# Performance work log

Hardware: AMD Instinct MI355X
Metric: run time of the kernel (lower is better)

## Reference

```python
import jax, jax.numpy as jnp
import numpy as np

M, K1, N1, N2, N3 = 131072, 256, 1024, 1024, 256


def setup_inputs() -> dict:
    key = jax.random.key(0)
    k_x, k1, k2, k3 = jax.random.split(key, 4)
    x = jax.random.normal(k_x, (M, K1), dtype=jnp.float32)
    # Kaiming-ish scaling so softplus stays in a sane range
    w1 = jax.random.normal(k1, (K1, N1), dtype=jnp.float32) * (1.0 / np.sqrt(K1))
    w2 = jax.random.normal(k2, (N1, N2), dtype=jnp.float32) * (1.0 / np.sqrt(N1))
    w3 = jax.random.normal(k3, (N2, N3), dtype=jnp.float32) * (1.0 / np.sqrt(N2))
    return {"x": x, "w1": w1, "w2": w2, "w3": w3}


def reference(x, w1, w2, w3):
    # Fused 3-layer MLP: out = softplus(softplus(x @ W1) @ W2) @ W3
    h1 = jax.nn.softplus(x @ w1)   # [M, N1]
    h2 = jax.nn.softplus(h1 @ w2)  # [M, N2]
    return h2 @ w3                 # [M, N3]
```

## Files before the change

### kernel.cpp

```cpp
#include <hip/hip_runtime.h>

typedef __attribute__((ext_vector_type(8))) short short8;
typedef __attribute__((ext_vector_type(4))) float floatx4;
typedef __attribute__((ext_vector_type(2))) unsigned int uintx2;
typedef __attribute__((ext_vector_type(4))) unsigned int uintx4;
typedef unsigned short u16;

#define MFMA(a, b, c) __builtin_amdgcn_mfma_f32_16x16x32_bf16((a), (b), (c), 0, 0, 0)
#define BAR() do { asm volatile("" ::: "memory"); __builtin_amdgcn_s_barrier(); \
                   asm volatile("" ::: "memory"); } while (0)
#define LGKM0() asm volatile("s_waitcnt lgkmcnt(0)" ::: "memory")

__device__ __forceinline__ u16 f2bf(float f) {
  unsigned int u = __builtin_bit_cast(unsigned int, f);
  u += ((u >> 16) & 1u) + 0x7fffu;
  return (u16)(u >> 16);
}

__device__ __forceinline__ float softplus_f(float v) {
  float a = __builtin_fabsf(v);
  float e = __expf(-a);
  float l = __logf(1.0f + e);
  return __builtin_fmaxf(v, 0.0f) + l;
}

__device__ __forceinline__ unsigned int pack_sp(float lo, float hi) {
  return (unsigned int)f2bf(softplus_f(lo)) | ((unsigned int)f2bf(softplus_f(hi)) << 16);
}

__global__ void transpose_cvt(const float* __restrict__ in, u16* __restrict__ out, int K, int N) {
  __shared__ float tile[32][33];
  const int bn = blockIdx.x * 32, bk = blockIdx.y * 32;
  const int tx = threadIdx.x, ty = threadIdx.y;
#pragma unroll
  for (int i = 0; i < 32; i += 8)
    tile[ty + i][tx] = in[(size_t)(bk + ty + i) * N + bn + tx];
  __syncthreads();
#pragma unroll
  for (int i = 0; i < 32; i += 8)
    out[(size_t)(bn + ty + i) * K + bk + tx] = f2bf(tile[tx][ty + i]);
}

__device__ __forceinline__ void gld16(const void* g, void* l) {
  __builtin_amdgcn_global_load_lds((const __attribute__((address_space(1))) void*)g,
                                   (__attribute__((address_space(3))) void*)l, 16, 0, 0);
}

template <int K, int EPI, bool ACTF32>
__global__ __launch_bounds__(512, 2) void gemm8(const void* __restrict__ actv,
                                                const u16* __restrict__ wt,
                                                void* __restrict__ Cout, int N, int nbn) {
  constexpr int H = K / 64;
  __shared__ u16 lds[2 * 4 * 8192];
  u16* L = lds;
  const int tid = threadIdx.x, lane = tid & 63, wv = tid >> 6;
  const int l15 = lane & 15, g = lane >> 4;
  const int wvm = wv >> 2, wvn = wv & 3;
  const int nwg = gridDim.x, o = blockIdx.x;
  const int sw = (o & 7) * (nwg >> 3) + (o >> 3);
  const int bm = sw / nbn, bn = sw % nbn;
  const size_t am0 = (size_t)bm * 256;
  const size_t wn0 = (size_t)bn * 256;

  int afo[8], wfo[4];
#pragma unroll
  for (int mt = 0; mt < 8; ++mt) {
    const int r = mt * 16 + l15;
    afo[mt] = (r * 8 + (g ^ ((r >> 1) & 7))) * 8;
  }
#pragma unroll
  for (int nt = 0; nt < 4; ++nt) {
    const int r = (wvn & 1) * 64 + nt * 16 + l15;
    wfo[nt] = (r * 8 + (g ^ ((r >> 1) & 7))) * 8;
  }
  const int aHalf = wvm * 8192;
  const int wHalf = (2 + (wvn >> 1)) * 8192;

  int soff[2], sdst[2];
#pragma unroll
  for (int j = 0; j < 2; ++j) {
    const int s = j * 512 + tid;
    const int r = s >> 3, gg = (s & 7) ^ ((r >> 1) & 7);
    soff[j] = r * K + gg * 8;
    sdst[j] = s * 8;
  }
  const u16* actb = nullptr;
  const float* factb = nullptr;
  if constexpr (ACTF32) factb = (const float*)actv + am0 * K;
  else actb = (const u16*)actv + am0 * K;
  const u16* wtb = wt + wn0 * K;

#define STG_W(tt, hi)                                                                \
  { _Pragma("unroll") for (int j = 0; j < 2; ++j)                                    \
      gld16(wtb + (size_t)(hi)*128 * K + soff[j] + (tt)*64,                          \
            L + ((tt)&1) * 32768 + (2 + (hi)) * 8192 + sdst[j]); }
#define STG_AB(tt, hi)                                                               \
  { _Pragma("unroll") for (int j = 0; j < 2; ++j)                                    \
      gld16(actb + (size_t)(hi)*128 * K + soff[j] + (tt)*64,                         \
            L + ((tt)&1) * 32768 + (hi)*8192 + sdst[j]); }
#define STG_AF(tt, hi)                                                               \
  { floatx4 v0[2], v1[2];                                                            \
    _Pragma("unroll") for (int j = 0; j < 2; ++j) {                                  \
      const float* sp_ = factb + (size_t)(hi)*128 * K + soff[j] + (tt)*64;           \
      v0[j] = *(const floatx4*)sp_;                                                  \
      v1[j] = *(const floatx4*)(sp_ + 4);                                            \
    }                                                                                \
    _Pragma("unroll") for (int j = 0; j < 2; ++j) {                                  \
      uintx4 w_;                                                                     \
      w_.x = (unsigned)f2bf(v0[j].x) | ((unsigned)f2bf(v0[j].y) << 16);              \
      w_.y = (unsigned)f2bf(v0[j].z) | ((unsigned)f2bf(v0[j].w) << 16);              \
      w_.z = (unsigned)f2bf(v1[j].x) | ((unsigned)f2bf(v1[j].y) << 16);              \
      w_.w = (unsigned)f2bf(v1[j].z) | ((unsigned)f2bf(v1[j].w) << 16);              \
      *(uintx4*)(L + ((tt)&1) * 32768 + (hi)*8192 + sdst[j]) = w_;                   \
    } }
#define STG_A(tt, hi)                                                                \
  { if constexpr (ACTF32) STG_AF(tt, hi) else STG_AB(tt, hi) }

  floatx4 acc[4][8];
  const floatx4 z4 = {0.f, 0.f, 0.f, 0.f};
#pragma unroll
  for (int t = 0; t < 4; ++t)
#pragma unroll
    for (int mt = 0; mt < 8; ++mt) acc[t][mt] = z4;

  STG_W(0, 0) STG_W(0, 1) STG_A(0, 0) STG_A(0, 1)
  STG_A(1, 0) STG_A(1, 1)
  if constexpr (ACTF32) { asm volatile("s_waitcnt vmcnt(0)" ::: "memory"); LGKM0(); }
  else asm volatile("s_waitcnt vmcnt(4)" ::: "memory");
  BAR();

  short8 A0[8], A1[8], wf0, wf1;

#pragma unroll 1
  for (int t = 0; t < H; ++t) {
    const int cb = (t & 1) * 32768;
#pragma unroll
    for (int mt = 0; mt < 8; ++mt) A0[mt] = *(const short8*)(L + cb + aHalf + afo[mt]);
    wf0 = *(const short8*)(L + cb + wHalf + wfo[0]);
    wf1 = *(const short8*)(L + cb + wHalf + wfo[1]);
    if (t + 1 < H) STG_W(t + 1, 0)
    BAR(); LGKM0();
    __builtin_amdgcn_s_setprio(1);
#pragma unroll
    for (int mt = 0; mt < 8; ++mt) {
      acc[0][mt] = MFMA(wf0, A0[mt], acc[0][mt]);
      acc[1][mt] = MFMA(wf1, A0[mt], acc[1][mt]);
    }
    __builtin_amdgcn_s_setprio(0);
    BAR();
#pragma unroll
    for (int mt = 0; mt < 8; ++mt) A1[mt] = *(const short8*)(L + cb + aHalf + (afo[mt] ^ 32));
    wf0 = *(const short8*)(L + cb + wHalf + (wfo[0] ^ 32));
    wf1 = *(const short8*)(L + cb + wHalf + (wfo[1] ^ 32));
    if (t + 1 < H) STG_W(t + 1, 1)
    BAR(); LGKM0();
    __builtin_amdgcn_s_setprio(1);
#pragma unroll
    for (int mt = 0; mt < 8; ++mt) {
      acc[0][mt] = MFMA(wf0, A1[mt], acc[0][mt]);
      acc[1][mt] = MFMA(wf1, A1[mt], acc[1][mt]);
    }
    __builtin_amdgcn_s_setprio(0);
    BAR();
    wf0 = *(const short8*)(L + cb + wHalf + wfo[2]);
    wf1 = *(const short8*)(L + cb + wHalf + wfo[3]);
    if (t + 2 < H) STG_A(t + 2, 0)
    BAR(); LGKM0();
    __builtin_amdgcn_s_setprio(1);
#pragma unroll
    for (int mt = 0; mt < 8; ++mt) {
      acc[2][mt] = MFMA(wf0, A0[mt], acc[2][mt]);
      acc[3][mt] = MFMA(wf1, A0[mt], acc[3][mt]);
    }
    __builtin_amdgcn_s_setprio(0);
    BAR();
    wf0 = *(const short8*)(L + cb + wHalf + (wfo[2] ^ 32));
    wf1 = *(const short8*)(L + cb + wHalf + (wfo[3] ^ 32));
    if (t + 2 < H) STG_A(t + 2, 1)
    if (t < H - 2) asm volatile("s_waitcnt vmcnt(4)" ::: "memory");
    else if (t == H - 2) asm volatile("s_waitcnt vmcnt(0)" ::: "memory");
    BAR(); LGKM0();
    __builtin_amdgcn_s_setprio(1);
#pragma unroll
    for (int mt = 0; mt < 8; ++mt) {
      acc[2][mt] = MFMA(wf0, A1[mt], acc[2][mt]);
      acc[3][mt] = MFMA(wf1, A1[mt], acc[3][mt]);
    }
    __builtin_amdgcn_s_setprio(0);
    BAR();
  }
#undef STG_W
#undef STG_AB
#undef STG_AF
#undef STG_A

  __syncthreads();

  if constexpr (EPI == 0) {
    u16* cl = L;
#pragma unroll
    for (int t = 0; t < 4; ++t)
#pragma unroll
      for (int mt = 0; mt < 8; ++mt) {
        const int m = wvm * 128 + mt * 16 + l15;
        const int n0 = wvn * 64 + t * 16 + g * 4;
        const int j = n0 >> 3, hh = (n0 >> 2) & 1;
        uintx2 pk;
        pk.x = pack_sp(acc[t][mt].x, acc[t][mt].y);
        pk.y = pack_sp(acc[t][mt].z, acc[t][mt].w);
        *(uintx2*)(cl + m * 256 + ((j ^ (m & 7)) << 3) + (hh << 2)) = pk;
      }
    __syncthreads();
    u16* outp = (u16*)Cout;
#pragma unroll
    for (int i = 0; i < 16; ++i) {
      const int c = i * 512 + tid;
      const int m = c >> 5, j = c & 31;
      uintx4 v = *(const uintx4*)(cl + m * 256 + ((j ^ (m & 7)) << 3));
      *(uintx4*)(outp + (am0 + m) * N + wn0 + j * 8) = v;
    }
  } else {
    float* cf = (float*)L;
#pragma unroll
    for (int q = 0; q < 2; ++q) {
      if (q) __syncthreads();
      if (wvm == q) {
#pragma unroll
        for (int t = 0; t < 4; ++t)
#pragma unroll
          for (int mt = 0; mt < 8; ++mt) {
            const int m = mt * 16 + l15;
            const int p = (wvn * 64 + t * 16 + g * 4) >> 1;
            *(floatx4*)(cf + m * 256 + ((p ^ ((m & 7) << 1)) << 1)) = acc[t][mt];
          }
      }
      __syncthreads();
      float* outp = (float*)Cout;
#pragma unroll
      for (int i = 0; i < 16; ++i) {
        const int c = i * 512 + tid;
        const int m = c >> 6, cc = c & 63;
        const int p = cc * 2;
        floatx4 v = *(const floatx4*)(cf + m * 256 + ((p ^ ((m & 7) << 1)) << 1));
        *(floatx4*)(outp + (am0 + q * 128 + m) * N + wn0 + cc * 4) = v;
      }
    }
  }
}

__global__ __launch_bounds__(512, 2) void mlp3_fused(const float* __restrict__ x,
                                                     const u16* __restrict__ w1t,
                                                     const u16* __restrict__ w2t,
                                                     const u16* __restrict__ w3t,
                                                     float* __restrict__ out) {
  __shared__ u16 h1s[64 * 1024];
  __shared__ u16 xs[64 * 256];
  const int tid = threadIdx.x, lane = tid & 63, wv = tid >> 6;
  const int l15 = lane & 15, g = lane >> 4;
  const size_t m0 = (size_t)blockIdx.x * 64;
  const floatx4 z4 = {0.f, 0.f, 0.f, 0.f};
  {
    const float* xp = x + m0 * 256;
#pragma unroll
    for (int r = 0; r < 8; ++r) {
      int idx4 = r * 512 + tid;
      int m = idx4 >> 6, k = (idx4 & 63) << 2;
      floatx4 v = *(const floatx4*)(xp + m * 256 + k);
      uintx2 pk;
      pk.x = (unsigned)f2bf(v.x) | ((unsigned)f2bf(v.y) << 16);
      pk.y = (unsigned)f2bf(v.z) | ((unsigned)f2bf(v.w) << 16);
      *(uintx2*)(xs + ((m * 256 + k) ^ ((m & 7) << 3))) = pk;
    }
  }
  __syncthreads();
#pragma unroll 1
  for (int c = 0; c < 4; ++c) {
    floatx4 acc[2][4];
#pragma unroll
    for (int t = 0; t < 2; ++t)
#pragma unroll
      for (int mt = 0; mt < 4; ++mt) acc[t][mt] = z4;
    const u16* p0 = w1t + (size_t)(c * 256 + wv * 32 + l15) * 256;
#pragma unroll
    for (int ks = 0; ks < 8; ++ks) {
      const int k = ks * 32 + g * 8;
      short8 a0 = *(const short8*)(p0 + k);
      short8 a1 = *(const short8*)(p0 + 16 * 256 + k);
      short8 b0 = *(const short8*)(xs + (((0 * 16 + l15) * 256 + k) ^ ((l15 & 7) << 3)));
      short8 b1 = *(const short8*)(xs + (((1 * 16 + l15) * 256 + k) ^ ((l15 & 7) << 3)));
      short8 b2 = *(const short8*)(xs + (((2 * 16 + l15) * 256 + k) ^ ((l15 & 7) << 3)));
      short8 b3 = *(const short8*)(xs + (((3 * 16 + l15) * 256 + k) ^ ((l15 & 7) << 3)));
      acc[0][0] = MFMA(a0, b0, acc[0][0]); acc[0][1] = MFMA(a0, b1, acc[0][1]);
      acc[0][2] = MFMA(a0, b2, acc[0][2]); acc[0][3] = MFMA(a0, b3, acc[0][3]);
      acc[1][0] = MFMA(a1, b0, acc[1][0]); acc[1][1] = MFMA(a1, b1, acc[1][1]);
      acc[1][2] = MFMA(a1, b2, acc[1][2]); acc[1][3] = MFMA(a1, b3, acc[1][3]);
    }
#pragma unroll
    for (int t = 0; t < 2; ++t)
#pragma unroll
      for (int mt = 0; mt < 4; ++mt) {
        const int n1 = c * 256 + wv * 32 + t * 16 + g * 4;
        const int m = mt * 16 + l15;
        uintx2 pk;
        pk.x = pack_sp(acc[t][mt].x, acc[t][mt].y);
        pk.y = pack_sp(acc[t][mt].z, acc[t][mt].w);
        *(uintx2*)(h1s + ((m * 1024 + n1) ^ ((m & 7) << 3))) = pk;
      }
  }
  __syncthreads();
  floatx4 acc3[2][4];
#pragma unroll
  for (int t = 0; t < 2; ++t)
#pragma unroll
    for (int mt = 0; mt < 4; ++mt) acc3[t][mt] = z4;
#pragma unroll 1
  for (int c2 = 0; c2 < 4; ++c2) {
    floatx4 acc2[2][4];
#pragma unroll
    for (int t = 0; t < 2; ++t)
#pragma unroll
      for (int mt = 0; mt < 4; ++mt) acc2[t][mt] = z4;
    {
      const u16* p0 = w2t + (size_t)(c2 * 256 + wv * 32 + l15) * 1024;
#pragma unroll 4
      for (int ks = 0; ks < 32; ++ks) {
        const int k = ks * 32 + g * 8;
        short8 a0 = *(const short8*)(p0 + k);
        short8 a1 = *(const short8*)(p0 + 16 * 1024 + k);
        short8 b0 = *(const short8*)(h1s + (((0 * 16 + l15) * 1024 + k) ^ ((l15 & 7) << 3)));
        short8 b1 = *(const short8*)(h1s + (((1 * 16 + l15) * 1024 + k) ^ ((l15 & 7) << 3)));
        short8 b2 = *(const short8*)(h1s + (((2 * 16 + l15) * 1024 + k) ^ ((l15 & 7) << 3)));
        short8 b3 = *(const short8*)(h1s + (((3 * 16 + l15) * 1024 + k) ^ ((l15 & 7) << 3)));
        acc2[0][0] = MFMA(a0, b0, acc2[0][0]); acc2[0][1] = MFMA(a0, b1, acc2[0][1]);
        acc2[0][2] = MFMA(a0, b2, acc2[0][2]); acc2[0][3] = MFMA(a0, b3, acc2[0][3]);
        acc2[1][0] = MFMA(a1, b0, acc2[1][0]); acc2[1][1] = MFMA(a1, b1, acc2[1][1]);
        acc2[1][2] = MFMA(a1, b2, acc2[1][2]); acc2[1][3] = MFMA(a1, b3, acc2[1][3]);
      }
    }
    __syncthreads();
#pragma unroll
    for (int t = 0; t < 2; ++t)
#pragma unroll
      for (int mt = 0; mt < 4; ++mt) {
        const int n2l = wv * 32 + t * 16 + g * 4;
        const int m = mt * 16 + l15;
        uintx2 pk;
        pk.x = pack_sp(acc2[t][mt].x, acc2[t][mt].y);
        pk.y = pack_sp(acc2[t][mt].z, acc2[t][mt].w);
        *(uintx2*)(xs + ((m * 256 + n2l) ^ ((m & 7) << 3))) = pk;
      }
    __syncthreads();
    {
      const u16* p0 = w3t + (size_t)(wv * 32 + l15) * 1024 + c2 * 256;
#pragma unroll
      for (int ks = 0; ks < 8; ++ks) {
        const int k = ks * 32 + g * 8;
        short8 a0 = *(const short8*)(p0 + k);
        short8 a1 = *(const short8*)(p0 + 16 * 1024 + k);
        short8 b0 = *(const short8*)(xs + (((0 * 16 + l15) * 256 + k) ^ ((l15 & 7) << 3)));
        short8 b1 = *(const short8*)(xs + (((1 * 16 + l15) * 256 + k) ^ ((l15 & 7) << 3)));
        short8 b2 = *(const short8*)(xs + (((2 * 16 + l15) * 256 + k) ^ ((l15 & 7) << 3)));
        short8 b3 = *(const short8*)(xs + (((3 * 16 + l15) * 256 + k) ^ ((l15 & 7) << 3)));
        acc3[0][0] = MFMA(a0, b0, acc3[0][0]); acc3[0][1] = MFMA(a0, b1, acc3[0][1]);
        acc3[0][2] = MFMA(a0, b2, acc3[0][2]); acc3[0][3] = MFMA(a0, b3, acc3[0][3]);
        acc3[1][0] = MFMA(a1, b0, acc3[1][0]); acc3[1][1] = MFMA(a1, b1, acc3[1][1]);
        acc3[1][2] = MFMA(a1, b2, acc3[1][2]); acc3[1][3] = MFMA(a1, b3, acc3[1][3]);
      }
    }
  }
#pragma unroll
  for (int t = 0; t < 2; ++t)
#pragma unroll
    for (int mt = 0; mt < 4; ++mt) {
      const int n3 = wv * 32 + t * 16 + g * 4;
      const int m = mt * 16 + l15;
      *(floatx4*)(out + (m0 + m) * 256 + n3) = acc3[t][mt];
    }
}

extern "C" void kernel_launch(void* const* d_in, const int* in_sizes, int n_in,
                              void* d_out, int out_size, void* d_ws, size_t ws_size,
                              hipStream_t stream) {
  const float* x = (const float*)d_in[0];
  const float* w1 = (const float*)d_in[1];
  const float* w2 = (const float*)d_in[2];
  const float* w3 = (const float*)d_in[3];
  float* out = (float*)d_out;
  const size_t M = 131072;

  u16* w1t = (u16*)d_ws;
  u16* w2t = w1t + 1024 * 256;
  u16* w3t = w2t + 1024 * 1024;
  u16* bufA = w3t + 256 * 1024;
  const size_t weights_el = 1024 * 256 + 1024 * 1024 + 256 * 1024;

  size_t CM = 0;
  const size_t cands[4] = {32768, 16384, 8192, 4096};
  for (int i = 0; i < 4; ++i) {
    size_t need = (weights_el + 2 * cands[i] * 1024) * sizeof(u16);
    if (ws_size >= need) { CM = cands[i]; break; }
  }

  dim3 tb(32, 8);
  transpose_cvt<<<dim3(32, 8), tb, 0, stream>>>(w1, w1t, 256, 1024);
  transpose_cvt<<<dim3(32, 32), tb, 0, stream>>>(w2, w2t, 1024, 1024);
  transpose_cvt<<<dim3(8, 32), tb, 0, stream>>>(w3, w3t, 1024, 256);

  if (CM) {
    u16* bufB = bufA + CM * 1024;
    const int nchunk = (int)(M / CM);
    for (int ci = 0; ci < nchunk; ++ci) {
      const float* xc = x + (size_t)ci * CM * 256;
      float* oc = out + (size_t)ci * CM * 256;
      gemm8<256, 0, true><<<(int)(CM / 256) * 4, 512, 0, stream>>>(xc, w1t, bufA, 1024, 4);
      gemm8<1024, 0, false><<<(int)(CM / 256) * 4, 512, 0, stream>>>(bufA, w2t, bufB, 1024, 4);
      gemm8<1024, 1, false><<<(int)(CM / 256), 512, 0, stream>>>(bufB, w3t, oc, 256, 1);
    }
  } else {
    mlp3_fused<<<M / 64, 512, 0, stream>>>(x, w1t, w2t, w3t, out);
  }
}
```

Baseline: 708.7 us.

## Store activations and weights as pre-swizzled tile images for contiguous LDS staging

Weights and intermediate activations are rewritten into a tiled layout that matches the swizzled LDS order, so each GEMM stage copies contiguous 16KB blocks straight into LDS. The fp32-to-bf16 conversion of x moves out of the first GEMM into a separate cvt_ximg pass, and GEMM epilogues now write the next layer's tile layout directly. The goal is fully coalesced, direct global-to-LDS loads and a simpler load path. The cost is an extra conversion kernel per chunk, extra x write/read traffic, and more setup kernels for the weights.

Result: no change. 713.6 us (+0.7%).

```diff
diff --git a/kernel.cpp b/kernel.cpp
--- a/kernel.cpp
+++ b/kernel.cpp
@@ -41,15 +41,50 @@
     out[(size_t)(bn + ty + i) * K + bk + tx] = f2bf(tile[tx][ty + i]);
 }
 
+
+__global__ void make_wimg(const u16* __restrict__ wt, u16* __restrict__ img, int K, int H) {
+  const int b = blockIdx.x;
+  const int hi = b & 1, th = (b >> 1) % H, bn = (b >> 1) / H;
+  const int tid = threadIdx.x;
+#pragma unroll
+  for (int j = 0; j < 2; ++j) {
+    const int s = j * 512 + tid;
+    const int r = s >> 3, gg = s & 7;
+    const int k0 = th * 64 + ((gg ^ ((r >> 1) & 7)) << 3);
+    short8 v = *(const short8*)(wt + (size_t)(bn * 256 + hi * 128 + r) * K + k0);
+    *(short8*)(img + (size_t)b * 8192 + s * 8) = v;
+  }
+}
+
+__global__ void cvt_ximg(const float* __restrict__ x, u16* __restrict__ img) {
+  const int b = blockIdx.x;
+  const int hi = b & 1, th = (b >> 1) & 3, mi = b >> 3;
+  const int tid = threadIdx.x;
+#pragma unroll
+  for (int j = 0; j < 2; ++j) {
+    const int s = j * 512 + tid;
+    const int r = s >> 3, gg = s & 7;
+    const int k0 = th * 64 + ((gg ^ ((r >> 1) & 7)) << 3);
+    const float* p = x + (size_t)(mi * 256 + hi * 128 + r) * 256 + k0;
+    floatx4 a = *(const floatx4*)p, c = *(const floatx4*)(p + 4);
+    uintx4 w;
+    w.x = (unsigned)f2bf(a.x) | ((unsigned)f2bf(a.y) << 16);
+    w.y = (unsigned)f2bf(a.z) | ((unsigned)f2bf(a.w) << 16);
+    w.z = (unsigned)f2bf(c.x) | ((unsigned)f2bf(c.y) << 16);
+    w.w = (unsigned)f2bf(c.z) | ((unsigned)f2bf(c.w) << 16);
+    *(uintx4*)(img + (size_t)b * 8192 + s * 8) = w;
+  }
+}
+
 __device__ __forceinline__ void gld16(const void* g, void* l) {
   __builtin_amdgcn_global_load_lds((const __attribute__((address_space(1))) void*)g,
                                    (__attribute__((address_space(3))) void*)l, 16, 0, 0);
 }
 
-template <int K, int EPI, bool ACTF32>
-__global__ __launch_bounds__(512, 2) void gemm8(const void* __restrict__ actv,
-                                                const u16* __restrict__ wt,
-                                                void* __restrict__ Cout, int N, int nbn) {
+template <int K, int HOUT, int EPI>
+__global__ __launch_bounds__(512, 2) void gemm8i(const u16* __restrict__ actimg,
+                                                 const u16* __restrict__ wimg,
+                                                 void* __restrict__ Cout, int N, int nbn) {
   constexpr int H = K / 64;
   __shared__ u16 lds[2 * 4 * 8192];
   u16* L = lds;
@@ -59,8 +94,6 @@
   const int nwg = gridDim.x, o = blockIdx.x;
   const int sw = (o & 7) * (nwg >> 3) + (o >> 3);
   const int bm = sw / nbn, bn = sw % nbn;
-  const size_t am0 = (size_t)bm * 256;
-  const size_t wn0 = (size_t)bn * 256;
 
   int afo[8], wfo[4];
 #pragma unroll
@@ -76,45 +109,13 @@
   const int aHalf = wvm * 8192;
   const int wHalf = (2 + (wvn >> 1)) * 8192;
 
-  int soff[2], sdst[2];
-#pragma unroll
-  for (int j = 0; j < 2; ++j) {
-    const int s = j * 512 + tid;
-    const int r = s >> 3, gg = (s & 7) ^ ((r >> 1) & 7);
-    soff[j] = r * K + gg * 8;
-    sdst[j] = s * 8;
-  }
-  const u16* actb = nullptr;
-  const float* factb = nullptr;
-  if constexpr (ACTF32) factb = (const float*)actv + am0 * K;
-  else actb = (const u16*)actv + am0 * K;
-  const u16* wtb = wt + wn0 * K;
-
-#define STG_W(tt, hi)                                                                \
+  const u16* ab = actimg + (size_t)bm * H * 16384;
+  const u16* wb = wimg + (size_t)bn * H * 16384;
+
+#define STG(base, tt, hi, lh)                                                        \
   { _Pragma("unroll") for (int j = 0; j < 2; ++j)                                    \
-      gld16(wtb + (size_t)(hi)*128 * K + soff[j] + (tt)*64,                          \
-            L + ((tt)&1) * 32768 + (2 + (hi)) * 8192 + sdst[j]); }
-#define STG_AB(tt, hi)                                                               \
-  { _Pragma("unroll") for (int j = 0; j < 2; ++j)                                    \
-      gld16(actb + (size_t)(hi)*128 * K + soff[j] + (tt)*64,                         \
-            L + ((tt)&1) * 32768 + (hi)*8192 + sdst[j]); }
-#define STG_AF(tt, hi)                                                               \
-  { floatx4 v0[2], v1[2];                                                            \
-    _Pragma("unroll") for (int j = 0; j < 2; ++j) {                                  \
-      const float* sp_ = factb + (size_t)(hi)*128 * K + soff[j] + (tt)*64;           \
-      v0[j] = *(const floatx4*)sp_;                                                  \
-      v1[j] = *(const floatx4*)(sp_ + 4);                                            \
-    }                                                                                \
-    _Pragma("unroll") for (int j = 0; j < 2; ++j) {                                  \
-      uintx4 w_;                                                                     \
-      w_.x = (unsigned)f2bf(v0[j].x) | ((unsigned)f2bf(v0[j].y) << 16);              \
-      w_.y = (unsigned)f2bf(v0[j].z) | ((unsigned)f2bf(v0[j].w) << 16);              \
-      w_.z = (unsigned)f2bf(v1[j].x) | ((unsigned)f2bf(v1[j].y) << 16);              \
-      w_.w = (unsigned)f2bf(v1[j].z) | ((unsigned)f2bf(v1[j].w) << 16);              \
-      *(uintx4*)(L + ((tt)&1) * 32768 + (hi)*8192 + sdst[j]) = w_;                   \
-    } }
-#define STG_A(tt, hi)                                                                \
-  { if constexpr (ACTF32) STG_AF(tt, hi) else STG_AB(tt, hi) }
+      gld16(base + ((size_t)(tt)*2 + (hi)) * 8192 + (j * 512 + tid) * 8,             \
+            L + ((tt)&1) * 32768 + (lh)*8192 + (j * 512 + tid) * 8); }
 
   floatx4 acc[4][8];
   const floatx4 z4 = {0.f, 0.f, 0.f, 0.f};
@@ -123,10 +124,9 @@
 #pragma unroll
     for (int mt = 0; mt < 8; ++mt) acc[t][mt] = z4;
 
-  STG_W(0, 0) STG_W(0, 1) STG_A(0, 0) STG_A(0, 1)
-  STG_A(1, 0) STG_A(1, 1)
-  if constexpr (ACTF32) { asm volatile("s_waitcnt vmcnt(0)" ::: "memory"); LGKM0(); }
-  else asm volatile("s_waitcnt vmcnt(4)" ::: "memory");
+  STG(ab, 0, 0, 0) STG(ab, 0, 1, 1) STG(wb, 0, 0, 2) STG(wb, 0, 1, 3)
+  STG(ab, 1, 0, 0) STG(ab, 1, 1, 1)
+  asm volatile("s_waitcnt vmcnt(4)" ::: "memory");
   BAR();
 
   short8 A0[8], A1[8], wf0, wf1;
@@ -138,7 +138,7 @@
     for (int mt = 0; mt < 8; ++mt) A0[mt] = *(const short8*)(L + cb + aHalf + afo[mt]);
     wf0 = *(const short8*)(L + cb + wHalf + wfo[0]);
     wf1 = *(const short8*)(L + cb + wHalf + wfo[1]);
-    if (t + 1 < H) STG_W(t + 1, 0)
+    if (t + 1 < H) STG(wb, t + 1, 0, 2)
     BAR(); LGKM0();
     __builtin_amdgcn_s_setprio(1);
 #pragma unroll
@@ -152,7 +152,7 @@
     for (int mt = 0; mt < 8; ++mt) A1[mt] = *(const short8*)(L + cb + aHalf + (afo[mt] ^ 32));
     wf0 = *(const short8*)(L + cb + wHalf + (wfo[0] ^ 32));
     wf1 = *(const short8*)(L + cb + wHalf + (wfo[1] ^ 32));
-    if (t + 1 < H) STG_W(t + 1, 1)
+    if (t + 1 < H) STG(wb, t + 1, 1, 3)
     BAR(); LGKM0();
     __builtin_amdgcn_s_setprio(1);
 #pragma unroll
@@ -164,7 +164,7 @@
     BAR();
     wf0 = *(const short8*)(L + cb + wHalf + wfo[2]);
     wf1 = *(const short8*)(L + cb + wHalf + wfo[3]);
-    if (t + 2 < H) STG_A(t + 2, 0)
+    if (t + 2 < H) STG(ab, t + 2, 0, 0)
     BAR(); LGKM0();
     __builtin_amdgcn_s_setprio(1);
 #pragma unroll
@@ -176,7 +176,7 @@
     BAR();
     wf0 = *(const short8*)(L + cb + wHalf + (wfo[2] ^ 32));
     wf1 = *(const short8*)(L + cb + wHalf + (wfo[3] ^ 32));
-    if (t + 2 < H) STG_A(t + 2, 1)
+    if (t + 2 < H) STG(ab, t + 2, 1, 1)
     if (t < H - 2) asm volatile("s_waitcnt vmcnt(4)" ::: "memory");
     else if (t == H - 2) asm volatile("s_waitcnt vmcnt(0)" ::: "memory");
     BAR(); LGKM0();
@@ -189,10 +189,7 @@
     __builtin_amdgcn_s_setprio(0);
     BAR();
   }
-#undef STG_W
-#undef STG_AB
-#undef STG_AF
-#undef STG_A
+#undef STG
 
   __syncthreads();
 
@@ -214,10 +211,14 @@
     u16* outp = (u16*)Cout;
 #pragma unroll
     for (int i = 0; i < 16; ++i) {
-      const int c = i * 512 + tid;
-      const int m = c >> 5, j = c & 31;
+      const int idx = i * 512 + tid;
+      const int t3 = idx >> 11, hi2 = (idx >> 10) & 1, s = idx & 1023;
+      const int r = s >> 3, gg = s & 7;
+      const int k64 = (gg ^ ((r >> 1) & 7)) << 3;
+      const int m = hi2 * 128 + r;
+      const int j = t3 * 8 + (k64 >> 3);
       uintx4 v = *(const uintx4*)(cl + m * 256 + ((j ^ (m & 7)) << 3));
-      *(uintx4*)(outp + (am0 + m) * N + wn0 + j * 8) = v;
+      *(uintx4*)(outp + ((size_t)(bm * HOUT + bn * 4 + t3) * 2 + hi2) * 8192 + s * 8) = v;
     }
   } else {
     float* cf = (float*)L;
@@ -242,7 +243,7 @@
         const int m = c >> 6, cc = c & 63;
         const int p = cc * 2;
         floatx4 v = *(const floatx4*)(cf + m * 256 + ((p ^ ((m & 7) << 1)) << 1));
-        *(floatx4*)(outp + (am0 + q * 128 + m) * N + wn0 + cc * 4) = v;
+        *(floatx4*)(outp + ((size_t)blockIdx.x * 0 + ((size_t)( (sw) / nbn) * 256 + q * 128 + m)) * N + (size_t)(sw % nbn) * 256 + cc * 4) = v;
       }
     }
   }
@@ -388,35 +389,46 @@
   float* out = (float*)d_out;
   const size_t M = 131072;
 
-  u16* w1t = (u16*)d_ws;
-  u16* w2t = w1t + 1024 * 256;
-  u16* w3t = w2t + 1024 * 1024;
-  u16* bufA = w3t + 256 * 1024;
-  const size_t weights_el = 1024 * 256 + 1024 * 1024 + 256 * 1024;
+  u16* wimg1 = (u16*)d_ws;
+  u16* wimg2 = wimg1 + 262144;
+  u16* wimg3 = wimg2 + 1048576;
+  u16* ximg = wimg3 + 262144;
 
   size_t CM = 0;
   const size_t cands[4] = {32768, 16384, 8192, 4096};
   for (int i = 0; i < 4; ++i) {
-    size_t need = (weights_el + 2 * cands[i] * 1024) * sizeof(u16);
+    size_t need = ((size_t)1572864 + cands[i] * 2304) * sizeof(u16);
     if (ws_size >= need) { CM = cands[i]; break; }
   }
 
   dim3 tb(32, 8);
-  transpose_cvt<<<dim3(32, 8), tb, 0, stream>>>(w1, w1t, 256, 1024);
-  transpose_cvt<<<dim3(32, 32), tb, 0, stream>>>(w2, w2t, 1024, 1024);
-  transpose_cvt<<<dim3(8, 32), tb, 0, stream>>>(w3, w3t, 1024, 256);
-
   if (CM) {
-    u16* bufB = bufA + CM * 1024;
+    u16* h1img = ximg + CM * 256;
+    u16* h2img = h1img + CM * 1024;
+    u16* tmp = ximg;
+    transpose_cvt<<<dim3(32, 8), tb, 0, stream>>>(w1, tmp, 256, 1024);
+    make_wimg<<<32, 512, 0, stream>>>(tmp, wimg1, 256, 4);
+    transpose_cvt<<<dim3(32, 32), tb, 0, stream>>>(w2, tmp, 1024, 1024);
+    make_wimg<<<128, 512, 0, stream>>>(tmp, wimg2, 1024, 16);
+    transpose_cvt<<<dim3(8, 32), tb, 0, stream>>>(w3, tmp, 1024, 256);
+    make_wimg<<<32, 512, 0, stream>>>(tmp, wimg3, 1024, 16);
+
     const int nchunk = (int)(M / CM);
     for (int ci = 0; ci < nchunk; ++ci) {
       const float* xc = x + (size_t)ci * CM * 256;
       float* oc = out + (size_t)ci * CM * 256;
-      gemm8<256, 0, true><<<(int)(CM / 256) * 4, 512, 0, stream>>>(xc, w1t, bufA, 1024, 4);
-      gemm8<1024, 0, false><<<(int)(CM / 256) * 4, 512, 0, stream>>>(bufA, w2t, bufB, 1024, 4);
-      gemm8<1024, 1, false><<<(int)(CM / 256), 512, 0, stream>>>(bufB, w3t, oc, 256, 1);
+      cvt_ximg<<<(int)(CM / 256) * 8, 512, 0, stream>>>(xc, ximg);
+      gemm8i<256, 16, 0><<<(int)(CM / 256) * 4, 512, 0, stream>>>(ximg, wimg1, h1img, 1024, 4);
+      gemm8i<1024, 16, 0><<<(int)(CM / 256) * 4, 512, 0, stream>>>(h1img, wimg2, h2img, 1024, 4);
+      gemm8i<1024, 0, 1><<<(int)(CM / 256), 512, 0, stream>>>(h2img, wimg3, oc, 256, 1);
     }
   } else {
+    u16* w1t = (u16*)d_ws;
+    u16* w2t = w1t + 1024 * 256;
+    u16* w3t = w2t + 1024 * 1024;
+    transpose_cvt<<<dim3(32, 8), tb, 0, stream>>>(w1, w1t, 256, 1024);
+    transpose_cvt<<<dim3(32, 32), tb, 0, stream>>>(w2, w2t, 1024, 1024);
+    transpose_cvt<<<dim3(8, 32), tb, 0, stream>>>(w3, w3t, 1024, 256);
     mlp3_fused<<<M / 64, 512, 0, stream>>>(x, w1t, w2t, w3t, out);
   }
 }
```
